# Performance work log

Hardware: AMD Instinct MI355X
Metric: run time of the kernel (lower is better)

## Reference

```python
import jax, jax.numpy as jnp
import numpy as np
from jax import lax

SCALE = 1.0
DENSE = 4
ITERS = 5


def setup_inputs() -> dict:
    key = jax.random.key(0)
    k1, k2, k3 = jax.random.split(key, 3)
    N, C, H, W = 32, 3, 512, 512
    A = 512
    data = jax.random.normal(k1, (N, C, H, W), dtype=jnp.float32)
    attx = jax.random.uniform(k2, (N, A), dtype=jnp.float32)
    atty = jax.random.uniform(k3, (N, A), dtype=jnp.float32)
    return {"data": data, "attx": attx, "atty": atty}


def _water_fill(attx, atty, out_size, out_sizey, in_size):
    # iterative water-filling clamp: 5 sequential max/min/sum/update passes
    att_size = attx.shape[1]
    att_sizey = atty.shape[1]
    thr0 = (SCALE * DENSE * in_size) / att_size
    ax = attx * out_size
    ay = atty * out_sizey
    for j in range(ITERS):
        mx = jnp.max(ax, axis=1, keepdims=True)
        my = jnp.max(ay, axis=1, keepdims=True)
        thr = jnp.minimum(mx, my)
        if j == 0:
            thr = jnp.minimum(thr, thr0)
        ax = jnp.minimum(ax, thr)
        ay = jnp.minimum(ay, thr)
        ax = ax + (out_size - jnp.sum(ax, axis=1, keepdims=True)) / att_size
        ay = ay + (out_sizey - jnp.sum(ay, axis=1, keepdims=True)) / att_sizey
    # as in the source: first element forced to 1 before cumsum
    ax = ax.at[:, 0].set(1.0)
    ay = ay.at[:, 0].set(1.0)
    return jnp.cumsum(ax, axis=1), jnp.cumsum(ay, axis=1), ax, ay


def _coords(att, cs, out_n):
    # inverse-CDF mapping: for each of out_n uniform steps of the sampled axis,
    # find the source bin in cumsum cs and interpolate -> coord in [-1,1]
    A = att.shape[1]
    step = cs[:, -1] / out_n                                   # (N,)
    t = jnp.arange(1, out_n + 1, dtype=cs.dtype)[None, :] * step[:, None]  # (N,out_n)

    def per_sample(cs_n, att_n, t_n):
        j = jnp.clip(jnp.searchsorted(cs_n, t_n, side='left'), 0, A - 1)
        prev = jnp.where(j > 0, cs_n[jnp.maximum(j - 1, 0)], 0.0)
        frac = (t_n - prev) / jnp.maximum(att_n[j], 1e-12)
        return (j.astype(cs_n.dtype) + frac) / A * 2.0 - 1.0

    return jax.vmap(per_sample)(cs, att, t)


def _grid_sample(data, grid):
    # F.grid_sample, bilinear, padding_mode='zeros', align_corners=False
    N, C, H, W = data.shape
    x = (grid[..., 0] + 1.0) * (W / 2.0) - 0.5   # (N,Ho,Wo)
    y = (grid[..., 1] + 1.0) * (H / 2.0) - 0.5
    x0 = jnp.floor(x)
    y0 = jnp.floor(y)
    x1 = x0 + 1.0
    y1 = y0 + 1.0
    wx1 = x - x0
    wx0 = 1.0 - wx1
    wy1 = y - y0
    wy0 = 1.0 - wy1

    def gather(ix, iy):
        valid = (ix >= 0) & (ix < W) & (iy >= 0) & (iy < H)
        ixc = jnp.clip(ix, 0, W - 1).astype(jnp.int32)
        iyc = jnp.clip(iy, 0, H - 1).astype(jnp.int32)
        v = jax.vmap(lambda d, iy_n, ix_n: d[:, iy_n, ix_n])(data, iyc, ixc)  # (N,C,Ho,Wo)
        return v * valid[:, None, :, :].astype(data.dtype)

    out = (gather(x0, y0) * (wx0 * wy0)[:, None]
           + gather(x1, y0) * (wx1 * wy0)[:, None]
           + gather(x0, y1) * (wx0 * wy1)[:, None]
           + gather(x1, y1) * (wx1 * wy1)[:, None])
    return out


def reference(data, attx, atty):
    N, C, H, W = data.shape
    out_size = int(H * SCALE)
    out_sizey = int(W * SCALE)
    # grid is built from detached attention (data.detach()/att.detach() in source)
    ax_ = lax.stop_gradient(attx)
    ay_ = lax.stop_gradient(atty)
    csx, csy, ax, ay = _water_fill(ax_, ay_, out_size, out_sizey, H)
    gy = _coords(ax, csx, out_size)    # height coords, (N,out_size)
    gx = _coords(ay, csy, out_sizey)   # width coords,  (N,out_sizey)
    grid = jnp.stack([
        jnp.broadcast_to(gx[:, None, :], (N, out_size, out_sizey)),
        jnp.broadcast_to(gy[:, :, None], (N, out_size, out_sizey)),
    ], axis=-1)  # (N,Ho,Wo,2)
    grid = lax.stop_gradient(grid)
    sampled = _grid_sample(data, grid)
    return sampled, grid
```

## Files before the change

kernel.cpp:

```cpp
#include <hip/hip_runtime.h>
#include <hip/hip_bf16.h>

#define AN 512
#define NB 32
#define HW 512

__device__ __forceinline__ float waveMax(float v) {
    #pragma unroll
    for (int off = 32; off > 0; off >>= 1) v = fmaxf(v, __shfl_xor(v, off, 64));
    return v;
}
__device__ __forceinline__ float waveSum(float v) {
    #pragma unroll
    for (int off = 32; off > 0; off >>= 1) v += __shfl_xor(v, off, 64);
    return v;
}

__global__ __launch_bounds__(512) void waterfill_coords_kernel(
    const float* __restrict__ attx, const float* __restrict__ atty,
    float* __restrict__ gx, float* __restrict__ gy)
{
    __shared__ float axs[AN], ays[AN], csx[AN], csy[AN];
    __shared__ float wmx[8], wmy[8], wsx[8], wsy[8], wtx[8], wty[8];
    const int n = blockIdx.x;
    const int t = threadIdx.x;
    const int wid = t >> 6;
    const int lane = t & 63;

    float ax = attx[n * AN + t] * 512.0f;
    float ay = atty[n * AN + t] * 512.0f;

    #pragma unroll
    for (int j = 0; j < 5; ++j) {
        float mx = waveMax(ax), my = waveMax(ay);
        if (lane == 0) { wmx[wid] = mx; wmy[wid] = my; }
        __syncthreads();
        float Mx = wmx[0], My = wmy[0];
        #pragma unroll
        for (int i = 1; i < 8; ++i) { Mx = fmaxf(Mx, wmx[i]); My = fmaxf(My, wmy[i]); }
        float thr = fminf(Mx, My);
        if (j == 0) thr = fminf(thr, 4.0f);
        ax = fminf(ax, thr);
        ay = fminf(ay, thr);

        float sx = waveSum(ax), sy = waveSum(ay);
        if (lane == 0) { wsx[wid] = sx; wsy[wid] = sy; }
        __syncthreads();
        float Sx = 0.0f, Sy = 0.0f;
        #pragma unroll
        for (int i = 0; i < 8; ++i) { Sx += wsx[i]; Sy += wsy[i]; }
        ax += (512.0f - Sx) * (1.0f / 512.0f);
        ay += (512.0f - Sy) * (1.0f / 512.0f);
    }

    if (t == 0) { ax = 1.0f; ay = 1.0f; }
    axs[t] = ax; ays[t] = ay;

    float cx = ax, cy = ay;
    #pragma unroll
    for (int off = 1; off < 64; off <<= 1) {
        float ux = __shfl_up(cx, off, 64);
        float uy = __shfl_up(cy, off, 64);
        if (lane >= off) { cx += ux; cy += uy; }
    }
    if (lane == 63) { wtx[wid] = cx; wty[wid] = cy; }
    __syncthreads();
    float px = 0.0f, py = 0.0f;
    #pragma unroll
    for (int i = 0; i < 8; ++i) {
        if (i < wid) { px += wtx[i]; py += wty[i]; }
    }
    cx += px; cy += py;
    csx[t] = cx; csy[t] = cy;
    __syncthreads();

    const float stepx = csx[AN - 1] * (1.0f / 512.0f);
    const float stepy = csy[AN - 1] * (1.0f / 512.0f);
    const float tvx = (float)(t + 1) * stepx;
    const float tvy = (float)(t + 1) * stepy;
    int lox = 0, hix = AN, loy = 0, hiy = AN;
    #pragma unroll
    for (int s = 0; s < 9; ++s) {
        const int mx_ = (lox + hix) >> 1;
        const int my_ = (loy + hiy) >> 1;
        const float vx = csx[mx_];
        const float vy = csy[my_];
        if (vx < tvx) lox = mx_ + 1; else hix = mx_;
        if (vy < tvy) loy = my_ + 1; else hiy = my_;
    }
    if (lox < hix && csx[lox] < tvx) ++lox;
    if (loy < hiy && csy[loy] < tvy) ++loy;
    {
        const int j = lox > (AN - 1) ? (AN - 1) : lox;
        const float prev = (j > 0) ? csx[j - 1] : 0.0f;
        const float frac = (tvx - prev) / fmaxf(axs[j], 1e-12f);
        gy[n * AN + t] = ((float)j + frac) * (2.0f / 512.0f) - 1.0f;
    }
    {
        const int j = loy > (AN - 1) ? (AN - 1) : loy;
        const float prev = (j > 0) ? csy[j - 1] : 0.0f;
        const float frac = (tvy - prev) / fmaxf(ays[j], 1e-12f);
        gx[n * AN + t] = ((float)j + frac) * (2.0f / 512.0f) - 1.0f;
    }
}

__global__ __launch_bounds__(256) void grid_sample_kernel(
    const float* __restrict__ data, const float* __restrict__ gx,
    const float* __restrict__ gy, float* __restrict__ outS,
    float* __restrict__ outG)
{
    __shared__ __align__(16) float rows[6][HW];
    const int t   = threadIdx.x;
    const int lid = blockIdx.x;
    const int wg  = (lid & 7) * 2048 + (lid >> 3);
    const int n   = wg >> 9;
    const int ho  = wg & 511;
    const int wid = t >> 6;
    const int lane = t & 63;

    const float gyv = gy[n * AN + ho];
    const float y   = (gyv + 1.0f) * 256.0f - 0.5f;
    const float y0f = floorf(y);
    const float wy1 = y - y0f, wy0 = 1.0f - wy1;
    const float vy0 = ((y0f >= 0.0f) & (y0f < 512.0f)) ? 1.0f : 0.0f;
    const float vy1 = ((y0f >= -1.0f) & (y0f < 511.0f)) ? 1.0f : 0.0f;
    const int y0 = (int)fminf(fmaxf(y0f, 0.0f), 511.0f);
    const int y1 = (int)fminf(fmaxf(y0f + 1.0f, 0.0f), 511.0f);

    const float* base = data + (size_t)n * 3 * HW * HW;
    #pragma unroll
    for (int r = 0; r < 3; ++r) {
        const int idx0 = r * 256 + (wid << 6);
        const int row0 = idx0 >> 7;
        const int col0 = idx0 & 127;
        const int yy   = (row0 < 3) ? y0 : y1;
        const int c    = (row0 < 3) ? row0 : row0 - 3;
        const float* g = base + ((size_t)c * HW + yy) * HW + ((col0 + lane) << 2);
        __builtin_amdgcn_global_load_lds(
            (const __attribute__((address_space(1))) void*)g,
            (__attribute__((address_space(3))) void*)(&rows[row0][col0 << 2]),
            16, 0, 0);
    }
    __syncthreads();

    const float2 gx2 = ((const float2*)(gx + n * AN))[t];
    const float xg[2] = {gx2.x, gx2.y};
    float res[3][2];

    #pragma unroll
    for (int k = 0; k < 2; ++k) {
        const float gxv = xg[k];
        const float x   = (gxv + 1.0f) * 256.0f - 0.5f;
        const float x0f = floorf(x);
        const float wx1 = x - x0f, wx0 = 1.0f - wx1;
        const float vx0 = ((x0f >= 0.0f) & (x0f < 512.0f)) ? 1.0f : 0.0f;
        const float vx1 = ((x0f >= -1.0f) & (x0f < 511.0f)) ? 1.0f : 0.0f;
        const int x0 = (int)fminf(fmaxf(x0f, 0.0f), 511.0f);
        const int x1 = (int)fminf(fmaxf(x0f + 1.0f, 0.0f), 511.0f);
        const float w00 = wx0 * wy0 * vx0 * vy0;
        const float w10 = wx1 * wy0 * vx1 * vy0;
        const float w01 = wx0 * wy1 * vx0 * vy1;
        const float w11 = wx1 * wy1 * vx1 * vy1;
        #pragma unroll
        for (int c = 0; c < 3; ++c) {
            res[c][k] = rows[c][x0] * w00 + rows[c][x1] * w10
                      + rows[3 + c][x0] * w01 + rows[3 + c][x1] * w11;
        }
    }

    const int wo = 2 * t;
    const size_t o = (((size_t)n * 3) * HW + ho) * HW + wo;
    #pragma unroll
    for (int c = 0; c < 3; ++c)
        *(float2*)(outS + o + (size_t)c * HW * HW) = make_float2(res[c][0], res[c][1]);

    *(float4*)(outG + (((size_t)n * HW + ho) * HW + wo) * 2) =
        make_float4(gx2.x, gyv, gx2.y, gyv);
}

extern "C" void kernel_launch(void* const* d_in, const int* in_sizes, int n_in,
                              void* d_out, int out_size, void* d_ws, size_t ws_size,
                              hipStream_t stream) {
    const float* data = (const float*)d_in[0];
    const float* attx = (const float*)d_in[1];
    const float* atty = (const float*)d_in[2];

    float* gx = (float*)d_ws;
    float* gy = gx + NB * AN;

    float* outS = (float*)d_out;
    float* outG = outS + (size_t)NB * 3 * HW * HW;

    waterfill_coords_kernel<<<NB, AN, 0, stream>>>(attx, atty, gx, gy);

    grid_sample_kernel<<<NB * HW, 256, 0, stream>>>(data, gx, gy, outS, outG);
}
```

Measured before the change: 250.1 us.

## Run waterfill on single wave with 8 elems per lane; pad LDS rows

The waterfill/coords kernel now uses one 64-lane wave per sample, with each lane holding 8 elements. This removes the block-wide __syncthreads reductions and turns the scan into a per-lane serial prefix plus one wave scan. The binary searches run serially, 8 per lane, which is more work per thread and less parallelism. In grid_sample, the LDS rows are padded to 516 with zeroed tails so each x1 read becomes xb+1 with a select, removing one clamp.

```diff
diff --git a/kernel.cpp b/kernel.cpp
--- a/kernel.cpp
+++ b/kernel.cpp
@@ -4,6 +4,7 @@
 #define AN 512
 #define NB 32
 #define HW 512
+#define RSTRIDE 516
 
 __device__ __forceinline__ float waveMax(float v) {
     #pragma unroll
@@ -16,91 +17,103 @@
     return v;
 }
 
-__global__ __launch_bounds__(512) void waterfill_coords_kernel(
+__global__ __launch_bounds__(64) void waterfill_coords_kernel(
     const float* __restrict__ attx, const float* __restrict__ atty,
     float* __restrict__ gx, float* __restrict__ gy)
 {
     __shared__ float axs[AN], ays[AN], csx[AN], csy[AN];
-    __shared__ float wmx[8], wmy[8], wsx[8], wsy[8], wtx[8], wty[8];
     const int n = blockIdx.x;
-    const int t = threadIdx.x;
-    const int wid = t >> 6;
-    const int lane = t & 63;
-
-    float ax = attx[n * AN + t] * 512.0f;
-    float ay = atty[n * AN + t] * 512.0f;
+    const int lane = threadIdx.x;
+    const int b = lane << 3;
+
+    float ax[8], ay[8];
+    {
+        const float4 x0 = ((const float4*)(attx + n * AN + b))[0];
+        const float4 x1 = ((const float4*)(attx + n * AN + b))[1];
+        const float4 y0 = ((const float4*)(atty + n * AN + b))[0];
+        const float4 y1 = ((const float4*)(atty + n * AN + b))[1];
+        ax[0] = x0.x * 512.0f; ax[1] = x0.y * 512.0f; ax[2] = x0.z * 512.0f; ax[3] = x0.w * 512.0f;
+        ax[4] = x1.x * 512.0f; ax[5] = x1.y * 512.0f; ax[6] = x1.z * 512.0f; ax[7] = x1.w * 512.0f;
+        ay[0] = y0.x * 512.0f; ay[1] = y0.y * 512.0f; ay[2] = y0.z * 512.0f; ay[3] = y0.w * 512.0f;
+        ay[4] = y1.x * 512.0f; ay[5] = y1.y * 512.0f; ay[6] = y1.z * 512.0f; ay[7] = y1.w * 512.0f;
+    }
 
     #pragma unroll
     for (int j = 0; j < 5; ++j) {
-        float mx = waveMax(ax), my = waveMax(ay);
-        if (lane == 0) { wmx[wid] = mx; wmy[wid] = my; }
-        __syncthreads();
-        float Mx = wmx[0], My = wmy[0];
-        #pragma unroll
-        for (int i = 1; i < 8; ++i) { Mx = fmaxf(Mx, wmx[i]); My = fmaxf(My, wmy[i]); }
-        float thr = fminf(Mx, My);
+        float mx = ax[0], my = ay[0];
+        #pragma unroll
+        for (int i = 1; i < 8; ++i) { mx = fmaxf(mx, ax[i]); my = fmaxf(my, ay[i]); }
+        mx = waveMax(mx); my = waveMax(my);
+        float thr = fminf(mx, my);
         if (j == 0) thr = fminf(thr, 4.0f);
-        ax = fminf(ax, thr);
-        ay = fminf(ay, thr);
-
-        float sx = waveSum(ax), sy = waveSum(ay);
-        if (lane == 0) { wsx[wid] = sx; wsy[wid] = sy; }
-        __syncthreads();
-        float Sx = 0.0f, Sy = 0.0f;
-        #pragma unroll
-        for (int i = 0; i < 8; ++i) { Sx += wsx[i]; Sy += wsy[i]; }
-        ax += (512.0f - Sx) * (1.0f / 512.0f);
-        ay += (512.0f - Sy) * (1.0f / 512.0f);
-    }
-
-    if (t == 0) { ax = 1.0f; ay = 1.0f; }
-    axs[t] = ax; ays[t] = ay;
-
-    float cx = ax, cy = ay;
+        float sx = 0.0f, sy = 0.0f;
+        #pragma unroll
+        for (int i = 0; i < 8; ++i) {
+            ax[i] = fminf(ax[i], thr); ay[i] = fminf(ay[i], thr);
+            sx += ax[i]; sy += ay[i];
+        }
+        sx = waveSum(sx); sy = waveSum(sy);
+        const float dx = (512.0f - sx) * (1.0f / 512.0f);
+        const float dy = (512.0f - sy) * (1.0f / 512.0f);
+        #pragma unroll
+        for (int i = 0; i < 8; ++i) { ax[i] += dx; ay[i] += dy; }
+    }
+
+    if (lane == 0) { ax[0] = 1.0f; ay[0] = 1.0f; }
+
+    float cxl[8], cyl[8];
+    float rx = 0.0f, ry = 0.0f;
+    #pragma unroll
+    for (int i = 0; i < 8; ++i) { rx += ax[i]; cxl[i] = rx; ry += ay[i]; cyl[i] = ry; }
+    float tx = rx, ty = ry;
     #pragma unroll
     for (int off = 1; off < 64; off <<= 1) {
-        float ux = __shfl_up(cx, off, 64);
-        float uy = __shfl_up(cy, off, 64);
-        if (lane >= off) { cx += ux; cy += uy; }
-    }
-    if (lane == 63) { wtx[wid] = cx; wty[wid] = cy; }
-    __syncthreads();
-    float px = 0.0f, py = 0.0f;
+        const float ux = __shfl_up(tx, off, 64);
+        const float uy = __shfl_up(ty, off, 64);
+        if (lane >= off) { tx += ux; ty += uy; }
+    }
+    const float ex = tx - rx, ey = ty - ry;
+    #pragma unroll
+    for (int i = 0; i < 8; ++i) { cxl[i] += ex; cyl[i] += ey; }
+
+    const float lastx = __shfl(tx, 63, 64);
+    const float lasty = __shfl(ty, 63, 64);
+
     #pragma unroll
     for (int i = 0; i < 8; ++i) {
-        if (i < wid) { px += wtx[i]; py += wty[i]; }
-    }
-    cx += px; cy += py;
-    csx[t] = cx; csy[t] = cy;
-    __syncthreads();
-
-    const float stepx = csx[AN - 1] * (1.0f / 512.0f);
-    const float stepy = csy[AN - 1] * (1.0f / 512.0f);
-    const float tvx = (float)(t + 1) * stepx;
-    const float tvy = (float)(t + 1) * stepy;
-    int lox = 0, hix = AN, loy = 0, hiy = AN;
-    #pragma unroll
-    for (int s = 0; s < 9; ++s) {
-        const int mx_ = (lox + hix) >> 1;
-        const int my_ = (loy + hiy) >> 1;
-        const float vx = csx[mx_];
-        const float vy = csy[my_];
-        if (vx < tvx) lox = mx_ + 1; else hix = mx_;
-        if (vy < tvy) loy = my_ + 1; else hiy = my_;
-    }
-    if (lox < hix && csx[lox] < tvx) ++lox;
-    if (loy < hiy && csy[loy] < tvy) ++loy;
-    {
-        const int j = lox > (AN - 1) ? (AN - 1) : lox;
-        const float prev = (j > 0) ? csx[j - 1] : 0.0f;
-        const float frac = (tvx - prev) / fmaxf(axs[j], 1e-12f);
-        gy[n * AN + t] = ((float)j + frac) * (2.0f / 512.0f) - 1.0f;
-    }
-    {
-        const int j = loy > (AN - 1) ? (AN - 1) : loy;
-        const float prev = (j > 0) ? csy[j - 1] : 0.0f;
-        const float frac = (tvy - prev) / fmaxf(ays[j], 1e-12f);
-        gx[n * AN + t] = ((float)j + frac) * (2.0f / 512.0f) - 1.0f;
+        axs[b + i] = ax[i]; ays[b + i] = ay[i];
+        csx[b + i] = cxl[i]; csy[b + i] = cyl[i];
+    }
+
+    const float stepx = lastx * (1.0f / 512.0f);
+    const float stepy = lasty * (1.0f / 512.0f);
+    float oy[8], ox[8];
+    #pragma unroll
+    for (int i = 0; i < 8; ++i) {
+        const int t = b + i;
+        const float tvx = (float)(t + 1) * stepx;
+        const float tvy = (float)(t + 1) * stepy;
+        int lox = 0, hix = AN, loy = 0, hiy = AN;
+        #pragma unroll
+        for (int s = 0; s < 9; ++s) {
+            const int mx_ = (lox + hix) >> 1;
+            const int my_ = (loy + hiy) >> 1;
+            if (csx[mx_] < tvx) lox = mx_ + 1; else hix = mx_;
+            if (csy[my_] < tvy) loy = my_ + 1; else hiy = my_;
+        }
+        if (lox < hix && csx[lox] < tvx) ++lox;
+        if (loy < hiy && csy[loy] < tvy) ++loy;
+        const int jx = lox > (AN - 1) ? (AN - 1) : lox;
+        const int jy = loy > (AN - 1) ? (AN - 1) : loy;
+        const float prevx = (jx > 0) ? csx[jx - 1] : 0.0f;
+        const float prevy = (jy > 0) ? csy[jy - 1] : 0.0f;
+        oy[i] = ((float)jx + (tvx - prevx) / fmaxf(axs[jx], 1e-12f)) * (2.0f / 512.0f) - 1.0f;
+        ox[i] = ((float)jy + (tvy - prevy) / fmaxf(ays[jy], 1e-12f)) * (2.0f / 512.0f) - 1.0f;
+    }
+    #pragma unroll
+    for (int i = 0; i < 8; ++i) {
+        gy[n * AN + b + i] = oy[i];
+        gx[n * AN + b + i] = ox[i];
     }
 }
 
@@ -109,7 +122,7 @@
     const float* __restrict__ gy, float* __restrict__ outS,
     float* __restrict__ outG)
 {
-    __shared__ __align__(16) float rows[6][HW];
+    __shared__ __align__(16) float rows[6][RSTRIDE];
     const int t   = threadIdx.x;
     const int lid = blockIdx.x;
     const int wg  = (lid & 7) * 2048 + (lid >> 3);
@@ -141,6 +154,7 @@
             (__attribute__((address_space(3))) void*)(&rows[row0][col0 << 2]),
             16, 0, 0);
     }
+    if (t < 24) rows[t >> 2][512 + (t & 3)] = 0.0f;
     __syncthreads();
 
     const float2 gx2 = ((const float2*)(gx + n * AN))[t];
@@ -155,16 +169,19 @@
         const float wx1 = x - x0f, wx0 = 1.0f - wx1;
         const float vx0 = ((x0f >= 0.0f) & (x0f < 512.0f)) ? 1.0f : 0.0f;
         const float vx1 = ((x0f >= -1.0f) & (x0f < 511.0f)) ? 1.0f : 0.0f;
-        const int x0 = (int)fminf(fmaxf(x0f, 0.0f), 511.0f);
-        const int x1 = (int)fminf(fmaxf(x0f + 1.0f, 0.0f), 511.0f);
+        const int xb = (int)fminf(fmaxf(x0f, 0.0f), 511.0f);
+        const bool lo_ok = (x0f >= 0.0f);
         const float w00 = wx0 * wy0 * vx0 * vy0;
         const float w10 = wx1 * wy0 * vx1 * vy0;
         const float w01 = wx0 * wy1 * vx0 * vy1;
         const float w11 = wx1 * wy1 * vx1 * vy1;
         #pragma unroll
         for (int c = 0; c < 3; ++c) {
-            res[c][k] = rows[c][x0] * w00 + rows[c][x1] * w10
-                      + rows[3 + c][x0] * w01 + rows[3 + c][x1] * w11;
+            const float a0 = rows[c][xb],     a1 = rows[c][xb + 1];
+            const float b0 = rows[3 + c][xb], b1 = rows[3 + c][xb + 1];
+            const float v10 = lo_ok ? a1 : a0;
+            const float v11 = lo_ok ? b1 : b0;
+            res[c][k] = a0 * w00 + v10 * w10 + b0 * w01 + v11 * w11;
         }
     }
 
@@ -191,7 +208,7 @@
     float* outS = (float*)d_out;
     float* outG = outS + (size_t)NB * 3 * HW * HW;
 
-    waterfill_coords_kernel<<<NB, AN, 0, stream>>>(attx, atty, gx, gy);
+    waterfill_coords_kernel<<<NB, 64, 0, stream>>>(attx, atty, gx, gy);
 
     grid_sample_kernel<<<NB * HW, 256, 0, stream>>>(data, gx, gy, outS, outG);
 }
```

Measured after the change: 253.6 us. No clear change (+1.4%).
